# Optimization experiments

Measured on AMD Instinct MI355X. Metric: run time of the kernel, lower is better.

The kernel has to match this reference:

```python
import jax, jax.numpy as jnp
import numpy as np

N_NODES = 50000
N_EDGES = 800000
NODE_IN_DIM = 768
NODE_DIM = 512
OUTPUT_NUM = 97
B, P = 8, 2048


def setup_inputs() -> dict:
    key = jax.random.key(0)
    ks = jax.random.split(key, 10)
    node_features = jax.random.normal(ks[0], (N_NODES, NODE_IN_DIM), jnp.float32)
    edge_features = jax.random.normal(ks[1], (N_EDGES, 32), jnp.float32)
    src = jax.random.randint(ks[2], (N_EDGES,), 0, N_NODES)
    dst = jax.random.randint(ks[3], (N_EDGES,), 0, N_NODES)
    head_ent_nodes = jax.random.randint(ks[4], (B, P), 0, N_NODES)
    tail_ent_nodes = jax.random.randint(ks[5], (B, P), 0, N_NODES)
    # params (xavier-ish scale for weights)
    W1 = jax.random.normal(ks[6], (NODE_IN_DIM, NODE_DIM), jnp.float32) / np.sqrt(NODE_IN_DIM)
    b1 = jax.random.normal(ks[7], (NODE_DIM,), jnp.float32) * 0.01
    Wp = jax.random.normal(ks[8], (2 * NODE_DIM, OUTPUT_NUM), jnp.float32) / np.sqrt(2 * NODE_DIM)
    bp = jax.random.normal(ks[9], (OUTPUT_NUM,), jnp.float32) * 0.01
    return {
        "node_features": node_features, "edge_features": edge_features,
        "W1": W1, "b1": b1, "Wp": Wp, "bp": bp,
        "src": src, "dst": dst,
        "head_ent_nodes": head_ent_nodes, "tail_ent_nodes": tail_ent_nodes,
    }


def reference(node_features, edge_features, W1, b1, Wp, bp, src, dst, head_ent_nodes, tail_ent_nodes):
    n = node_features.shape[0]
    # node_fc: Linear + ReLU
    h = jax.nn.relu(node_features @ W1 + b1)  # [N, D]
    # DGL update_all: message = dst node's own h, mean-reduced at dst.
    # (src is part of the graph but unused by this message function.)
    msg = h[dst]  # [E, D] gather
    agg = jax.ops.segment_sum(msg, dst, num_segments=n)  # [N, D]
    deg = jax.ops.segment_sum(jnp.ones((dst.shape[0],), h.dtype), dst, num_segments=n)  # [N]
    # nodes with no incoming messages keep their old h (DGL UDF semantics)
    h_new = jnp.where((deg > 0)[:, None], agg / jnp.maximum(deg, 1.0)[:, None], h)
    head = h_new[head_ent_nodes]  # [B, P, D]
    tail = h_new[tail_ent_nodes]  # [B, P, D]
    out = jnp.concatenate([head, tail], axis=2) @ Wp + bp  # [B, P, 97]
    return out
```

## Files before the change

### kernel.cpp

```cpp
#include <hip/hip_runtime.h>
#include <hip/hip_bf16.h>
#include <stdint.h>

using bf16x8 = __attribute__((ext_vector_type(8))) short;
using f32x4  = __attribute__((ext_vector_type(4))) float;

#define N_NODES  50000
#define K1       768
#define D1       512
#define NPAIR    16384
#define NOUT     97
#define NOUT_PAD 112
#define MTILES   391
#define NTILES   4
#define NWG      (MTILES * NTILES)
#define WGPX     196
#define KSTEPS   (K1 / 32)

__device__ __forceinline__ uint16_t f2bf(float f) {
    uint32_t u = __builtin_bit_cast(uint32_t, f);
    return (uint16_t)((u + 0x7fffu + ((u >> 16) & 1u)) >> 16);
}

__device__ __forceinline__ uint32_t cvt_pk_bf16(float lo, float hi) {
    uint32_t r;
    asm("v_cvt_pk_bf16_f32 %0, %1, %2" : "=v"(r) : "v"(lo), "v"(hi));
    return r;
}

__device__ __forceinline__ void gll16(const void* g, void* l) {
    __builtin_amdgcn_global_load_lds(
        (const __attribute__((address_space(1))) void*)g,
        (__attribute__((address_space(3))) void*)l, 16, 0, 0);
}

__global__ void k_convert(const float* __restrict__ W1, const float* __restrict__ Wp,
                          uint16_t* __restrict__ W1t, uint16_t* __restrict__ Wpt) {
    int idx = blockIdx.x * 256 + threadIdx.x;
    const int n1 = D1 * K1;
    if (idx < n1) {
        int c = idx / K1, k = idx - c * K1;
        W1t[idx] = f2bf(W1[k * D1 + c]);
    } else {
        int j = idx - n1;
        if (j < NOUT_PAD * 1024) {
            int c = j >> 10, k = j & 1023;
            Wpt[j] = (c < NOUT) ? f2bf(Wp[k * NOUT + c]) : (uint16_t)0;
        }
    }
}

__global__ __launch_bounds__(256) void k_gemm1(const float* __restrict__ A,
        const uint16_t* __restrict__ W1t, const float* __restrict__ bias1,
        uint16_t* __restrict__ H) {
    __shared__ float    lds_a[2 * 4096];
    __shared__ uint16_t lds_b[2 * 4096];

    const int bid = blockIdx.x;
    const int tt = (bid & 7) * WGPX + (bid >> 3);
    if (tt >= NWG) return;
    const int m0 = (tt >> 2) * 128, n0 = (tt & 3) * 128;

    const int t = threadIdx.x, lane = t & 63, w = t >> 6;
    const int wm = w >> 1, wn = w & 1;
    const int cl = lane & 15, kh = lane >> 4;
    const int l3 = lane >> 3, l7 = lane & 7;

    const float* aSrc[4];
    #pragma unroll
    for (int i = 0; i < 4; ++i) {
        int r = m0 + w * 32 + i * 8 + l3;
        if (r >= N_NODES) r = N_NODES - 1;
        aSrc[i] = A + (size_t)r * K1 + ((l7 ^ l3) * 4);
    }
    const uint16_t* bSrc[2];
    #pragma unroll
    for (int i = 0; i < 2; ++i)
        bSrc[i] = W1t + (size_t)(n0 + w * 32 + i * 16 + (lane >> 2)) * K1
                      + (((lane & 3) ^ ((lane >> 3) & 3)) * 8);

    float*    aDst = &lds_a[w * 1024];
    uint16_t* bDst = &lds_b[w * 1024];

    const int q7 = cl & 7;
    const int pa0 = ((2 * kh) ^ q7) * 4, pa1 = ((2 * kh + 1) ^ q7) * 4;
    const int arow0 = (wm * 64 + cl) * 32;
    const int brow0 = (wn * 64 + cl) * 32 + ((kh ^ ((cl >> 1) & 3)) * 8);

    f32x4 acc[4][4];
    const f32x4 z = {0.f, 0.f, 0.f, 0.f};
    #pragma unroll
    for (int m = 0; m < 4; ++m)
        #pragma unroll
        for (int n = 0; n < 4; ++n) acc[m][n] = z;

#define STAGE(BUF) do {                                                    \
    _Pragma("unroll")                                                      \
    for (int i = 0; i < 4; ++i) gll16(aSrc[i], aDst + (BUF) * 4096 + i * 256); \
    _Pragma("unroll")                                                      \
    for (int i = 0; i < 2; ++i) gll16(bSrc[i], bDst + (BUF) * 4096 + i * 512); \
    _Pragma("unroll")                                                      \
    for (int i = 0; i < 4; ++i) aSrc[i] += 32;                             \
    _Pragma("unroll")                                                      \
    for (int i = 0; i < 2; ++i) bSrc[i] += 32;                             \
    } while (0)

#define COMPUTE(BUF) do {                                                  \
    const float*    la = &lds_a[(BUF) * 4096];                             \
    const uint16_t* lb = &lds_b[(BUF) * 4096];                             \
    bf16x8 af[4], bfr[4];                                                  \
    _Pragma("unroll")                                                      \
    for (int n = 0; n < 4; ++n)                                            \
        bfr[n] = *(const bf16x8*)&lb[brow0 + n * 512];                     \
    _Pragma("unroll")                                                      \
    for (int m = 0; m < 4; ++m) {                                          \
        f32x4 r0 = *(const f32x4*)&la[arow0 + m * 512 + pa0];              \
        f32x4 r1 = *(const f32x4*)&la[arow0 + m * 512 + pa1];              \
        uint32_t uu[4];                                                    \
        uu[0] = cvt_pk_bf16(r0[0], r0[1]);                                 \
        uu[1] = cvt_pk_bf16(r0[2], r0[3]);                                 \
        uu[2] = cvt_pk_bf16(r1[0], r1[1]);                                 \
        uu[3] = cvt_pk_bf16(r1[2], r1[3]);                                 \
        af[m] = *(const bf16x8*)uu;                                        \
    }                                                                      \
    _Pragma("unroll")                                                      \
    for (int m = 0; m < 4; ++m)                                            \
        _Pragma("unroll")                                                  \
        for (int n = 0; n < 4; ++n)                                        \
            acc[m][n] = __builtin_amdgcn_mfma_f32_16x16x32_bf16(           \
                            af[m], bfr[n], acc[m][n], 0, 0, 0);            \
    } while (0)

    STAGE(0);
    for (int kt = 0; kt < KSTEPS - 1; ++kt) {
        const int cur = kt & 1;
        STAGE(cur ^ 1);
        asm volatile("s_waitcnt vmcnt(6)" ::: "memory");
        __builtin_amdgcn_s_barrier();
        COMPUTE(cur);
        __builtin_amdgcn_s_barrier();
    }
    asm volatile("s_waitcnt vmcnt(0)" ::: "memory");
    __builtin_amdgcn_s_barrier();
    COMPUTE((KSTEPS - 1) & 1);

#undef STAGE
#undef COMPUTE

    float bv[4]; int bcol[4];
    #pragma unroll
    for (int n = 0; n < 4; ++n) { bcol[n] = n0 + wn * 64 + n * 16 + cl; bv[n] = bias1[bcol[n]]; }
    #pragma unroll
    for (int m = 0; m < 4; ++m) {
        int rbase = m0 + wm * 64 + m * 16 + kh * 4;
        #pragma unroll
        for (int rr = 0; rr < 4; ++rr) {
            int row = rbase + rr;
            if (row < N_NODES) {
                #pragma unroll
                for (int n = 0; n < 4; ++n) {
                    float v = acc[m][n][rr] + bv[n];
                    H[(size_t)row * D1 + bcol[n]] = f2bf(fmaxf(v, 0.f));
                }
            }
        }
    }
}

__global__ __launch_bounds__(256) void k_gemm2(const uint16_t* __restrict__ H,
        const uint16_t* __restrict__ Wpt, const float* __restrict__ bp,
        const int* __restrict__ head, const int* __restrict__ tail,
        float* __restrict__ out) {
    __shared__ uint16_t lds_w[NOUT_PAD][40];
    const int t = threadIdx.x;
    const int lane = t & 63, wave = t >> 6;
    const int cl = lane & 15, kh = lane >> 4;
    const int rowbase = blockIdx.x * 64 + wave * 16;
    const int i_l = rowbase + cl;
    const int nodeH = head[i_l], nodeT = tail[i_l];
    const uint16_t* hH = H + (size_t)nodeH * D1 + kh * 8;
    const uint16_t* hT = H + (size_t)nodeT * D1 + kh * 8;

    f32x4 acc[7];
    const f32x4 z = {0.f, 0.f, 0.f, 0.f};
    #pragma unroll
    for (int n = 0; n < 7; ++n) acc[n] = z;

    const int wrow = t >> 1, whalf = t & 1;
    const uint16_t* wsrc = Wpt + (size_t)wrow * 1024 + whalf * 16;
    uint16_t* wdst = &lds_w[wrow][whalf * 16];

    for (int kb = 0; kb < 32; ++kb) {
        uint4 w0 = {0,0,0,0}, w1 = {0,0,0,0};
        if (t < 224) {
            const uint4* wp4 = (const uint4*)(wsrc + kb * 32);
            w0 = wp4[0]; w1 = wp4[1];
        }
        bf16x8 af = (kb < 16) ? *(const bf16x8*)(hH + kb * 32)
                              : *(const bf16x8*)(hT + (kb - 16) * 32);
        __syncthreads();
        if (t < 224) { ((uint4*)wdst)[0] = w0; ((uint4*)wdst)[1] = w1; }
        __syncthreads();
        #pragma unroll
        for (int n = 0; n < 7; ++n) {
            bf16x8 bfr = *(const bf16x8*)&lds_w[n * 16 + cl][kh * 8];
            acc[n] = __builtin_amdgcn_mfma_f32_16x16x32_bf16(af, bfr, acc[n], 0, 0, 0);
        }
    }
    #pragma unroll
    for (int n = 0; n < 7; ++n) {
        int col = n * 16 + cl;
        if (col < NOUT) {
            float bb = bp[col];
            #pragma unroll
            for (int rr = 0; rr < 4; ++rr) {
                int i = rowbase + kh * 4 + rr;
                out[(size_t)i * NOUT + col] = acc[n][rr] + bb;
            }
        }
    }
}

extern "C" void kernel_launch(void* const* d_in, const int* in_sizes, int n_in,
                              void* d_out, int out_size, void* d_ws, size_t ws_size,
                              hipStream_t stream) {
    const float* node_features = (const float*)d_in[0];
    const float* W1   = (const float*)d_in[2];
    const float* b1   = (const float*)d_in[3];
    const float* Wp   = (const float*)d_in[4];
    const float* bp   = (const float*)d_in[5];
    const int* head   = (const int*)d_in[8];
    const int* tail   = (const int*)d_in[9];
    float* out = (float*)d_out;

    char* ws = (char*)d_ws;
    uint16_t* H   = (uint16_t*)ws;
    uint16_t* W1t = (uint16_t*)(ws + (size_t)N_NODES * D1 * 2);
    uint16_t* Wpt = (uint16_t*)(ws + (size_t)N_NODES * D1 * 2 + (size_t)D1 * K1 * 2);

    const int convN = D1 * K1 + NOUT_PAD * 1024;
    k_convert<<<(convN + 255) / 256, 256, 0, stream>>>(W1, Wp, W1t, Wpt);

    k_gemm1<<<WGPX * 8, 256, 0, stream>>>(node_features, W1t, b1, H);

    k_gemm2<<<NPAIR / 64, 256, 0, stream>>>(H, Wpt, bp, head, tail, out);
}
```

Baseline: 109.9 us.

## Split gemm1 tile across eight waves with smaller per-wave M subtile

The first GEMM kernel now launches 512 threads (8 waves) per 128x128 tile instead of 256. Each wave computes a 32x64 subtile rather than 64x64, and the global-to-LDS staging is redistributed so each thread issues three loads per k-step instead of six. The intent is more waves to hide latency and fewer accumulator registers per thread, at the cost of less register reuse of B fragments and more LDS reads per MFMA.

```diff
diff --git a/kernel.cpp b/kernel.cpp
--- a/kernel.cpp
+++ b/kernel.cpp
@@ -50,7 +50,7 @@
     }
 }
 
-__global__ __launch_bounds__(256) void k_gemm1(const float* __restrict__ A,
+__global__ __launch_bounds__(512) void k_gemm1(const float* __restrict__ A,
         const uint16_t* __restrict__ W1t, const float* __restrict__ bias1,
         uint16_t* __restrict__ H) {
     __shared__ float    lds_a[2 * 4096];
@@ -64,78 +64,68 @@
     const int t = threadIdx.x, lane = t & 63, w = t >> 6;
     const int wm = w >> 1, wn = w & 1;
     const int cl = lane & 15, kh = lane >> 4;
-    const int l3 = lane >> 3, l7 = lane & 7;
-
-    const float* aSrc[4];
-    #pragma unroll
-    for (int i = 0; i < 4; ++i) {
-        int r = m0 + w * 32 + i * 8 + l3;
+
+    const float* aSrc[2];
+    #pragma unroll
+    for (int i = 0; i < 2; ++i) {
+        int r = m0 + i * 64 + (t >> 3);
         if (r >= N_NODES) r = N_NODES - 1;
-        aSrc[i] = A + (size_t)r * K1 + ((l7 ^ l3) * 4);
-    }
-    const uint16_t* bSrc[2];
-    #pragma unroll
-    for (int i = 0; i < 2; ++i)
-        bSrc[i] = W1t + (size_t)(n0 + w * 32 + i * 16 + (lane >> 2)) * K1
-                      + (((lane & 3) ^ ((lane >> 3) & 3)) * 8);
-
-    float*    aDst = &lds_a[w * 1024];
-    uint16_t* bDst = &lds_b[w * 1024];
+        aSrc[i] = A + (size_t)r * K1 + (((t & 7) ^ ((t >> 3) & 7)) * 4);
+    }
+    const uint16_t* bSrc =
+        W1t + (size_t)(n0 + (t >> 2)) * K1 + (((t & 3) ^ ((t >> 3) & 3)) * 8);
+
+    float*    aDst = &lds_a[w * 256];
+    uint16_t* bDst = &lds_b[w * 512];
 
     const int q7 = cl & 7;
     const int pa0 = ((2 * kh) ^ q7) * 4, pa1 = ((2 * kh + 1) ^ q7) * 4;
-    const int arow0 = (wm * 64 + cl) * 32;
+    const int arow0 = (wm * 32 + cl) * 32;
     const int brow0 = (wn * 64 + cl) * 32 + ((kh ^ ((cl >> 1) & 3)) * 8);
 
-    f32x4 acc[4][4];
+    f32x4 acc[2][4];
     const f32x4 z = {0.f, 0.f, 0.f, 0.f};
     #pragma unroll
-    for (int m = 0; m < 4; ++m)
+    for (int m = 0; m < 2; ++m)
         #pragma unroll
         for (int n = 0; n < 4; ++n) acc[m][n] = z;
 
-#define STAGE(BUF) do {                                                    \
-    _Pragma("unroll")                                                      \
-    for (int i = 0; i < 4; ++i) gll16(aSrc[i], aDst + (BUF) * 4096 + i * 256); \
-    _Pragma("unroll")                                                      \
-    for (int i = 0; i < 2; ++i) gll16(bSrc[i], bDst + (BUF) * 4096 + i * 512); \
-    _Pragma("unroll")                                                      \
-    for (int i = 0; i < 4; ++i) aSrc[i] += 32;                             \
-    _Pragma("unroll")                                                      \
-    for (int i = 0; i < 2; ++i) bSrc[i] += 32;                             \
+#define STAGE(BUF) do {                                                        \
+    gll16(aSrc[0], aDst + (BUF) * 4096);                                       \
+    gll16(aSrc[1], aDst + (BUF) * 4096 + 2048);                                \
+    gll16(bSrc,    bDst + (BUF) * 4096);                                       \
+    aSrc[0] += 32; aSrc[1] += 32; bSrc += 32;                                  \
     } while (0)
 
-#define COMPUTE(BUF) do {                                                  \
-    const float*    la = &lds_a[(BUF) * 4096];                             \
-    const uint16_t* lb = &lds_b[(BUF) * 4096];                             \
-    bf16x8 af[4], bfr[4];                                                  \
-    _Pragma("unroll")                                                      \
-    for (int n = 0; n < 4; ++n)                                            \
-        bfr[n] = *(const bf16x8*)&lb[brow0 + n * 512];                     \
-    _Pragma("unroll")                                                      \
-    for (int m = 0; m < 4; ++m) {                                          \
-        f32x4 r0 = *(const f32x4*)&la[arow0 + m * 512 + pa0];              \
-        f32x4 r1 = *(const f32x4*)&la[arow0 + m * 512 + pa1];              \
-        uint32_t uu[4];                                                    \
-        uu[0] = cvt_pk_bf16(r0[0], r0[1]);                                 \
-        uu[1] = cvt_pk_bf16(r0[2], r0[3]);                                 \
-        uu[2] = cvt_pk_bf16(r1[0], r1[1]);                                 \
-        uu[3] = cvt_pk_bf16(r1[2], r1[3]);                                 \
-        af[m] = *(const bf16x8*)uu;                                        \
-    }                                                                      \
-    _Pragma("unroll")                                                      \
-    for (int m = 0; m < 4; ++m)                                            \
-        _Pragma("unroll")                                                  \
-        for (int n = 0; n < 4; ++n)                                        \
-            acc[m][n] = __builtin_amdgcn_mfma_f32_16x16x32_bf16(           \
-                            af[m], bfr[n], acc[m][n], 0, 0, 0);            \
+#define COMPUTE(BUF) do {                                                      \
+    const float*    la = &lds_a[(BUF) * 4096];                                 \
+    const uint16_t* lb = &lds_b[(BUF) * 4096];                                 \
+    bf16x8 bfr[4];                                                             \
+    _Pragma("unroll")                                                          \
+    for (int n = 0; n < 4; ++n)                                                \
+        bfr[n] = *(const bf16x8*)&lb[brow0 + n * 512];                         \
+    _Pragma("unroll")                                                          \
+    for (int m = 0; m < 2; ++m) {                                              \
+        f32x4 r0 = *(const f32x4*)&la[arow0 + m * 512 + pa0];                  \
+        f32x4 r1 = *(const f32x4*)&la[arow0 + m * 512 + pa1];                  \
+        uint32_t uu[4];                                                        \
+        uu[0] = cvt_pk_bf16(r0[0], r0[1]);                                     \
+        uu[1] = cvt_pk_bf16(r0[2], r0[3]);                                     \
+        uu[2] = cvt_pk_bf16(r1[0], r1[1]);                                     \
+        uu[3] = cvt_pk_bf16(r1[2], r1[3]);                                     \
+        bf16x8 af = *(const bf16x8*)uu;                                        \
+        _Pragma("unroll")                                                      \
+        for (int n = 0; n < 4; ++n)                                            \
+            acc[m][n] = __builtin_amdgcn_mfma_f32_16x16x32_bf16(               \
+                            af, bfr[n], acc[m][n], 0, 0, 0);                   \
+    }                                                                          \
     } while (0)
 
     STAGE(0);
     for (int kt = 0; kt < KSTEPS - 1; ++kt) {
         const int cur = kt & 1;
         STAGE(cur ^ 1);
-        asm volatile("s_waitcnt vmcnt(6)" ::: "memory");
+        asm volatile("s_waitcnt vmcnt(3)" ::: "memory");
         __builtin_amdgcn_s_barrier();
         COMPUTE(cur);
         __builtin_amdgcn_s_barrier();
@@ -151,8 +141,8 @@
     #pragma unroll
     for (int n = 0; n < 4; ++n) { bcol[n] = n0 + wn * 64 + n * 16 + cl; bv[n] = bias1[bcol[n]]; }
     #pragma unroll
-    for (int m = 0; m < 4; ++m) {
-        int rbase = m0 + wm * 64 + m * 16 + kh * 4;
+    for (int m = 0; m < 2; ++m) {
+        int rbase = m0 + wm * 32 + m * 16 + kh * 4;
         #pragma unroll
         for (int rr = 0; rr < 4; ++rr) {
             int row = rbase + rr;
@@ -241,7 +231,7 @@
     const int convN = D1 * K1 + NOUT_PAD * 1024;
     k_convert<<<(convN + 255) / 256, 256, 0, stream>>>(W1, Wp, W1t, Wpt);
 
-    k_gemm1<<<WGPX * 8, 256, 0, stream>>>(node_features, W1t, b1, H);
+    k_gemm1<<<WGPX * 8, 512, 0, stream>>>(node_features, W1t, b1, H);
 
     k_gemm2<<<NPAIR / 64, 256, 0, stream>>>(H, Wpt, bp, head, tail, out);
 }
```

New measurement: 99.75 us. 1.1x faster.
